# Kernel optimization log

Hardware: AMD Instinct MI355X
Metric: run time of the kernel (lower is better)

The kernel has to match this reference:

```python
import jax, jax.numpy as jnp
import numpy as np


def setup_inputs() -> dict:
    key = jax.random.key(0)
    k1, k2 = jax.random.split(key)
    B, N, M, C = 4, 8192, 8192, 3
    ref = jax.random.normal(k1, (B, N, C), dtype=jnp.float32)
    query = jax.random.normal(k2, (B, M, C), dtype=jnp.float32)
    return {"ref": ref, "query": query, "k": 16}


def reference(ref, query, k):
    # ref:   [B, N, C] reference points
    # query: [B, M, C] query points
    # Squared Euclidean distances via ||q||^2 + ||r||^2 - 2 q.r  -> [B, M, N]
    q_sq = jnp.sum(query * query, axis=-1, keepdims=True)          # [B, M, 1]
    r_sq = jnp.sum(ref * ref, axis=-1)[:, None, :]                 # [B, 1, N]
    cross = jnp.einsum("bmc,bnc->bmn", query, ref)                 # [B, M, N]
    d2 = jnp.maximum(q_sq + r_sq - 2.0 * cross, 0.0)
    # k smallest distances, sorted ascending (knn_cuda convention)
    neg_topk, idx = jax.lax.top_k(-d2, k)                          # [B, M, k]
    dist = jnp.sqrt(-neg_topk)
    return dist, idx
```

## Files before the change

kernel.cpp:

```cpp
#include <hip/hip_runtime.h>


#define TPB 256
#define QPB 32
#define SPL 8
#define KK 16
#define TILE_PTS 512
#define CAP 16
#define TRIG 8

__global__ __launch_bounds__(TPB, 4) void knn_topk_kernel(
    const float* __restrict__ ref, const float* __restrict__ query,
    float* __restrict__ dout, float* __restrict__ iout, int N, int M) {
#pragma clang fp contract(off)
  __shared__ float4 tile[TILE_PTS];
  __shared__ unsigned short si[CAP * TPB];
  __shared__ float md[KK * TPB];

  const int tid = threadIdx.x;
  const int h = tid & (SPL - 1);
  const int qid = blockIdx.x * QPB + (tid >> 3);
  const int b = qid / M;

  const float* qp = query + (size_t)qid * 3;
  const float qx = qp[0], qy = qp[1], qz = qp[2];
  float q2 = (qx * qx + qz * qz) + qy * qy;

  float a[KK];
  int ai[KK];
#pragma unroll
  for (int s = 0; s < KK; ++s) { a[s] = 3.0e38f; ai[s] = 0; }
  float T = 3.0e38f;
  int cnt = 0;

  const float* refb = ref + (size_t)b * N * 3;

  auto insert16 = [&](float d, int ix) {
    bool pc = false;
    float pa = 0.f;
    int pi = 0;
#pragma unroll
    for (int s = 0; s < KK; ++s) {
      float oa = a[s];
      int oi = ai[s];
      bool c = d < oa;
      a[s] = c ? (pc ? pa : d) : oa;
      ai[s] = c ? (pc ? pi : ix) : oi;
      pc = c;
      pa = oa;
      pi = oi;
    }
  };

  auto compact = [&](int tbase) {
    int cm = cnt;
    for (int s = 0; s < cm; ++s) {
      int loc = si[s * TPB + tid];
      float4 p = tile[loc];
      float cr = qx * p.x;
      cr = __builtin_fmaf(qy, p.y, cr);
      cr = __builtin_fmaf(qz, p.z, cr);
      float s2 = q2 + p.w;
      float d2 = __builtin_fmaf(-2.0f, cr, s2);
      float d2c = d2 < 0.f ? 0.f : d2;
      if (d2c < a[KK - 1]) insert16(d2c, tbase + loc);
    }
    cnt = 0;
    float a15 = a[KK - 1];
    float m = fminf(a15, __shfl_xor(a15, 1));
    m = fminf(m, __shfl_xor(m, 2));
    T = fminf(m, __shfl_xor(m, 4));
  };

  const int ntiles = N / TILE_PTS;
  for (int t = 0; t < ntiles; ++t) {
    __syncthreads();
    {
      int pl = tid * 2;
      const float* rp = refb + (size_t)(t * TILE_PTS + pl) * 3;
#pragma unroll
      for (int u = 0; u < 2; ++u) {
        float rx = rp[3 * u + 0];
        float ry = rp[3 * u + 1];
        float rz = rp[3 * u + 2];
        float r2 = (rx * rx + rz * rz) + ry * ry;
        tile[pl + u] = make_float4(rx, ry, rz, r2);
      }
    }
    __syncthreads();
    const int tbase = t * TILE_PTS;
    for (int g = 0; g < TILE_PTS / SPL; g += 8) {
#pragma unroll
      for (int u = 0; u < 8; ++u) {
        const int loc = (g + u) * SPL + h;
        float4 p = tile[loc];
        float cr = qx * p.x;
        cr = __builtin_fmaf(qy, p.y, cr);
        cr = __builtin_fmaf(qz, p.z, cr);
        float s2 = q2 + p.w;
        float d2 = __builtin_fmaf(-2.0f, cr, s2);
        if (d2 <= T) {
          si[cnt * TPB + tid] = (unsigned short)loc;
          cnt++;
        }
      }
      if (__any(cnt >= TRIG)) compact(tbase);
    }
    if (__any(cnt > 0)) compact(tbase);
  }

#pragma unroll
  for (int s = 0; s < KK; ++s) {
    md[s * TPB + tid] = a[s];
    si[s * TPB + tid] = (unsigned short)ai[s];
  }
  __syncthreads();
  if (h == 0) {
    int pp[SPL];
    float hd[SPL];
    int hi[SPL];
#pragma unroll
    for (int j = 0; j < SPL; ++j) {
      pp[j] = 0;
      hd[j] = md[tid + j];
      hi[j] = si[tid + j];
    }
    float* dq = dout + (size_t)qid * KK;
    float* iq = iout + (size_t)qid * KK;
    for (int o = 0; o < KK; ++o) {
      int best = 0;
#pragma unroll
      for (int j = 1; j < SPL; ++j) {
        bool bt = (hd[j] < hd[best]) || (hd[j] == hd[best] && hi[j] < hi[best]);
        if (bt) best = j;
      }
      dq[o] = sqrtf(hd[best]);
      iq[o] = (float)hi[best];
      int np = pp[best] + 1;
      pp[best] = np;
      if (np < KK) {
        hd[best] = md[np * TPB + tid + best];
        hi[best] = si[np * TPB + tid + best];
      } else {
        hd[best] = 3.0e38f;
      }
    }
  }
}

extern "C" void kernel_launch(void* const* d_in, const int* in_sizes, int n_in,
                              void* d_out, int out_size, void* d_ws, size_t ws_size,
                              hipStream_t stream) {
  const float* ref = (const float*)d_in[0];
  const float* query = (const float*)d_in[1];
  const int B = 4, C = 3;
  int N = in_sizes[0] / (B * C);
  int M = in_sizes[1] / (B * C);
  float* dout = (float*)d_out;
  float* iout = dout + (size_t)out_size / 2;
  int totalQ = B * M;
  int blocks = totalQ / QPB;
  knn_topk_kernel<<<blocks, TPB, 0, stream>>>(ref, query, dout, iout, N, M);
}
```

Before: 285.6 us.

## Replace insertion top-k with packed 64-bit keys, sorting networks and shuffle merge

Top-k candidates become packed 64-bit (distance bits, index) keys. Buffered candidates are batch-sorted with a 16-element sorting network and bitonic-merged into the running list, replacing the per-candidate insertion and the recompute of distances. The list is seeded from the first 16 points, the 8 sub-lists are merged with warp shuffles instead of a shared-memory serial merge, and ref loads and output stores are vectorised with float4. Block size drops to 128 threads. The 64-bit keys raise register pressure, and indices are stored as unsigned short, which relies on N being at most 65536.

Measured after the change: 260.3 us, median of 2. 8.9% less time.

```diff
diff --git a/kernel.cpp b/kernel.cpp
--- a/kernel.cpp
+++ b/kernel.cpp
@@ -1,21 +1,56 @@
 #include <hip/hip_runtime.h>
 
 
-#define TPB 256
-#define QPB 32
+#define TPB 128
+#define QPB 16
 #define SPL 8
 #define KK 16
 #define TILE_PTS 512
 #define CAP 16
 #define TRIG 8
 
+typedef unsigned long long u64k;
+
+#define CE(x, i, j)                                   \
+  {                                                   \
+    u64k ki_ = x[i], kj_ = x[j];                      \
+    bool c_ = kj_ < ki_;                              \
+    x[i] = c_ ? kj_ : ki_;                            \
+    x[j] = c_ ? ki_ : kj_;                            \
+  }
+
+__device__ __forceinline__ void sort16(u64k x[KK]) {
+  CE(x,0,1) CE(x,2,3) CE(x,4,5) CE(x,6,7) CE(x,8,9) CE(x,10,11) CE(x,12,13) CE(x,14,15)
+  CE(x,0,2) CE(x,1,3) CE(x,4,6) CE(x,5,7) CE(x,8,10) CE(x,9,11) CE(x,12,14) CE(x,13,15)
+  CE(x,1,2) CE(x,5,6) CE(x,9,10) CE(x,13,14)
+  CE(x,0,4) CE(x,1,5) CE(x,2,6) CE(x,3,7) CE(x,8,12) CE(x,9,13) CE(x,10,14) CE(x,11,15)
+  CE(x,2,4) CE(x,3,5) CE(x,10,12) CE(x,11,13)
+  CE(x,1,2) CE(x,3,4) CE(x,5,6) CE(x,9,10) CE(x,11,12) CE(x,13,14)
+  CE(x,0,8) CE(x,1,9) CE(x,2,10) CE(x,3,11) CE(x,4,12) CE(x,5,13) CE(x,6,14) CE(x,7,15)
+  CE(x,4,8) CE(x,5,9) CE(x,6,10) CE(x,7,11)
+  CE(x,2,4) CE(x,3,5) CE(x,6,8) CE(x,7,9) CE(x,10,12) CE(x,11,13)
+  CE(x,1,2) CE(x,3,4) CE(x,5,6) CE(x,7,8) CE(x,9,10) CE(x,11,12) CE(x,13,14)
+}
+
+__device__ __forceinline__ void mergeTop16(u64k a[KK], u64k e[KK]) {
+#pragma unroll
+  for (int i = 0; i < KK; ++i) {
+    u64k bv = e[KK - 1 - i];
+    if (bv < a[i]) a[i] = bv;
+  }
+  CE(a,0,8) CE(a,1,9) CE(a,2,10) CE(a,3,11) CE(a,4,12) CE(a,5,13) CE(a,6,14) CE(a,7,15)
+  CE(a,0,4) CE(a,1,5) CE(a,2,6) CE(a,3,7) CE(a,8,12) CE(a,9,13) CE(a,10,14) CE(a,11,15)
+  CE(a,0,2) CE(a,1,3) CE(a,4,6) CE(a,5,7) CE(a,8,10) CE(a,9,11) CE(a,12,14) CE(a,13,15)
+  CE(a,0,1) CE(a,2,3) CE(a,4,5) CE(a,6,7) CE(a,8,9) CE(a,10,11) CE(a,12,13) CE(a,14,15)
+}
+
 __global__ __launch_bounds__(TPB, 4) void knn_topk_kernel(
     const float* __restrict__ ref, const float* __restrict__ query,
     float* __restrict__ dout, float* __restrict__ iout, int N, int M) {
 #pragma clang fp contract(off)
   __shared__ float4 tile[TILE_PTS];
-  __shared__ unsigned short si[CAP * TPB];
-  __shared__ float md[KK * TPB];
+  __shared__ unsigned int sd[CAP * TPB];
+  __shared__ unsigned short sg[CAP * TPB];
 
   const int tid = threadIdx.x;
   const int h = tid & (SPL - 1);
@@ -26,47 +61,25 @@
   const float qx = qp[0], qy = qp[1], qz = qp[2];
   float q2 = (qx * qx + qz * qz) + qy * qy;
 
-  float a[KK];
-  int ai[KK];
-#pragma unroll
-  for (int s = 0; s < KK; ++s) { a[s] = 3.0e38f; ai[s] = 0; }
-  float T = 3.0e38f;
+  u64k kl[KK];
+  float T;
   int cnt = 0;
 
   const float* refb = ref + (size_t)b * N * 3;
 
-  auto insert16 = [&](float d, int ix) {
-    bool pc = false;
-    float pa = 0.f;
-    int pi = 0;
+  auto compact = [&]() {
+    u64k e[KK];
 #pragma unroll
     for (int s = 0; s < KK; ++s) {
-      float oa = a[s];
-      int oi = ai[s];
-      bool c = d < oa;
-      a[s] = c ? (pc ? pa : d) : oa;
-      ai[s] = c ? (pc ? pi : ix) : oi;
-      pc = c;
-      pa = oa;
-      pi = oi;
+      unsigned int db = sd[s * TPB + tid];
+      unsigned int gi = sg[s * TPB + tid];
+      u64k key = ((u64k)db << 32) | gi;
+      e[s] = (s < cnt) ? key : ~0ull;
     }
-  };
-
-  auto compact = [&](int tbase) {
-    int cm = cnt;
-    for (int s = 0; s < cm; ++s) {
-      int loc = si[s * TPB + tid];
-      float4 p = tile[loc];
-      float cr = qx * p.x;
-      cr = __builtin_fmaf(qy, p.y, cr);
-      cr = __builtin_fmaf(qz, p.z, cr);
-      float s2 = q2 + p.w;
-      float d2 = __builtin_fmaf(-2.0f, cr, s2);
-      float d2c = d2 < 0.f ? 0.f : d2;
-      if (d2c < a[KK - 1]) insert16(d2c, tbase + loc);
-    }
+    sort16(e);
+    mergeTop16(kl, e);
     cnt = 0;
-    float a15 = a[KK - 1];
+    float a15 = __uint_as_float((unsigned)(kl[KK - 1] >> 32));
     float m = fminf(a15, __shfl_xor(a15, 1));
     m = fminf(m, __shfl_xor(m, 2));
     T = fminf(m, __shfl_xor(m, 4));
@@ -76,20 +89,42 @@
   for (int t = 0; t < ntiles; ++t) {
     __syncthreads();
     {
-      int pl = tid * 2;
-      const float* rp = refb + (size_t)(t * TILE_PTS + pl) * 3;
-#pragma unroll
-      for (int u = 0; u < 2; ++u) {
-        float rx = rp[3 * u + 0];
-        float ry = rp[3 * u + 1];
-        float rz = rp[3 * u + 2];
-        float r2 = (rx * rx + rz * rz) + ry * ry;
-        tile[pl + u] = make_float4(rx, ry, rz, r2);
-      }
+      int pl = tid * 4;
+      const float4* rp =
+          (const float4*)(refb + (size_t)(t * TILE_PTS + pl) * 3);
+      float4 f0 = rp[0], f1 = rp[1], f2 = rp[2];
+      float x0 = f0.x, y0 = f0.y, z0 = f0.z;
+      float x1 = f0.w, y1 = f1.x, z1 = f1.y;
+      float x2 = f1.z, y2 = f1.w, z2 = f2.x;
+      float x3 = f2.y, y3 = f2.z, z3 = f2.w;
+      tile[pl + 0] = make_float4(x0, y0, z0, (x0 * x0 + z0 * z0) + y0 * y0);
+      tile[pl + 1] = make_float4(x1, y1, z1, (x1 * x1 + z1 * z1) + y1 * y1);
+      tile[pl + 2] = make_float4(x2, y2, z2, (x2 * x2 + z2 * z2) + y2 * y2);
+      tile[pl + 3] = make_float4(x3, y3, z3, (x3 * x3 + z3 * z3) + y3 * y3);
     }
     __syncthreads();
     const int tbase = t * TILE_PTS;
-    for (int g = 0; g < TILE_PTS / SPL; g += 8) {
+    int g0 = 0;
+    if (t == 0) {
+#pragma unroll
+      for (int n = 0; n < KK; ++n) {
+        float4 p = tile[n * SPL + h];
+        float cr = qx * p.x;
+        cr = __builtin_fmaf(qy, p.y, cr);
+        cr = __builtin_fmaf(qz, p.z, cr);
+        float s2 = q2 + p.w;
+        float d2 = __builtin_fmaf(-2.0f, cr, s2);
+        float d2c = d2 < 0.f ? 0.f : d2;
+        kl[n] = ((u64k)__float_as_uint(d2c) << 32) | (unsigned)(n * SPL + h);
+      }
+      sort16(kl);
+      float a15 = __uint_as_float((unsigned)(kl[KK - 1] >> 32));
+      float m = fminf(a15, __shfl_xor(a15, 1));
+      m = fminf(m, __shfl_xor(m, 2));
+      T = fminf(m, __shfl_xor(m, 4));
+      g0 = 16;
+    }
+    for (int g = g0; g < TILE_PTS / SPL; g += 8) {
 #pragma unroll
       for (int u = 0; u < 8; ++u) {
         const int loc = (g + u) * SPL + h;
@@ -100,51 +135,42 @@
         float s2 = q2 + p.w;
         float d2 = __builtin_fmaf(-2.0f, cr, s2);
         if (d2 <= T) {
-          si[cnt * TPB + tid] = (unsigned short)loc;
+          float d2c = d2 < 0.f ? 0.f : d2;
+          sd[cnt * TPB + tid] = __float_as_uint(d2c);
+          sg[cnt * TPB + tid] = (unsigned short)(tbase + loc);
           cnt++;
         }
       }
-      if (__any(cnt >= TRIG)) compact(tbase);
+      if (__any(cnt >= TRIG)) compact();
     }
-    if (__any(cnt > 0)) compact(tbase);
+  }
+  if (__any(cnt > 0)) compact();
+
+#pragma unroll
+  for (int d = 1; d < SPL; d <<= 1) {
+    u64k r[KK];
+#pragma unroll
+    for (int s = 0; s < KK; ++s) r[s] = __shfl_xor(kl[s], d);
+    mergeTop16(kl, r);
   }
 
-#pragma unroll
-  for (int s = 0; s < KK; ++s) {
-    md[s * TPB + tid] = a[s];
-    si[s * TPB + tid] = (unsigned short)ai[s];
-  }
-  __syncthreads();
   if (h == 0) {
-    int pp[SPL];
-    float hd[SPL];
-    int hi[SPL];
-#pragma unroll
-    for (int j = 0; j < SPL; ++j) {
-      pp[j] = 0;
-      hd[j] = md[tid + j];
-      hi[j] = si[tid + j];
-    }
     float* dq = dout + (size_t)qid * KK;
     float* iq = iout + (size_t)qid * KK;
+    float dv[KK], iv[KK];
+#pragma unroll
     for (int o = 0; o < KK; ++o) {
-      int best = 0;
-#pragma unroll
-      for (int j = 1; j < SPL; ++j) {
-        bool bt = (hd[j] < hd[best]) || (hd[j] == hd[best] && hi[j] < hi[best]);
-        if (bt) best = j;
-      }
-      dq[o] = sqrtf(hd[best]);
-      iq[o] = (float)hi[best];
-      int np = pp[best] + 1;
-      pp[best] = np;
-      if (np < KK) {
-        hd[best] = md[np * TPB + tid + best];
-        hi[best] = si[np * TPB + tid + best];
-      } else {
-        hd[best] = 3.0e38f;
-      }
+      dv[o] = sqrtf(__uint_as_float((unsigned)(kl[o] >> 32)));
+      iv[o] = (float)(unsigned)(kl[o] & 0xffffffffu);
     }
+    ((float4*)dq)[0] = make_float4(dv[0], dv[1], dv[2], dv[3]);
+    ((float4*)dq)[1] = make_float4(dv[4], dv[5], dv[6], dv[7]);
+    ((float4*)dq)[2] = make_float4(dv[8], dv[9], dv[10], dv[11]);
+    ((float4*)dq)[3] = make_float4(dv[12], dv[13], dv[14], dv[15]);
+    ((float4*)iq)[0] = make_float4(iv[0], iv[1], iv[2], iv[3]);
+    ((float4*)iq)[1] = make_float4(iv[4], iv[5], iv[6], iv[7]);
+    ((float4*)iq)[2] = make_float4(iv[8], iv[9], iv[10], iv[11]);
+    ((float4*)iq)[3] = make_float4(iv[12], iv[13], iv[14], iv[15]);
   }
 }
 
```
